# Kernel optimization log

Hardware: AMD Instinct MI355X
Metric: run time of the kernel (lower is better)

## Reference

```python
import jax, jax.numpy as jnp
import numpy as np

N_NODES = 50000
N_EDGES = 800000
D = 128
L = 4
N_GRAPHS = 512
N_CLASSES = 10
BN_EPS = 1e-5


def setup_inputs() -> dict:
    key = jax.random.key(0)
    ks = jax.random.split(key, 8)
    x = jax.random.normal(ks[0], (N_NODES, D), dtype=jnp.float32)
    W = jax.random.normal(ks[1], (L, D, D), dtype=jnp.float32) * (1.0 / np.sqrt(D))
    b = jnp.zeros((L, D), dtype=jnp.float32)
    gamma = jnp.ones((L, D), dtype=jnp.float32)
    beta = jnp.zeros((L, D), dtype=jnp.float32)
    Wc = jax.random.normal(ks[2], (D, N_CLASSES), dtype=jnp.float32) * (1.0 / np.sqrt(D))
    bc = jnp.zeros((N_CLASSES,), dtype=jnp.float32)
    edge_index = jax.random.randint(ks[3], (2, N_EDGES), 0, N_NODES, dtype=jnp.int64)
    batch = jnp.sort(jax.random.randint(ks[4], (N_NODES,), 0, N_GRAPHS, dtype=jnp.int64))
    return {"x": x, "W": W, "b": b, "gamma": gamma, "beta": beta,
            "Wc": Wc, "bc": bc, "edge_index": edge_index, "batch": batch}


def _gcn_conv(x, W_l, b_l, src, dst, deg_inv, norm):
    # h = x @ W, then symmetric-normalized aggregation with self-loops (PyG GCNConv)
    h = x @ W_l                                            # [N, D]
    msg = h[src] * norm[:, None]                           # [E, D] gather + scale
    agg = jax.ops.segment_sum(msg, dst, num_segments=N_NODES)  # scatter-add
    agg = agg + h * (deg_inv * deg_inv)[:, None]           # self-loop term: deg^-1 * h_i
    return agg + b_l


def reference(x, W, b, gamma, beta, Wc, bc, edge_index, batch):
    src, dst = edge_index[0], edge_index[1]
    # degree with self-loops (edge_weight = 1), computed at target nodes
    deg = jax.ops.segment_sum(jnp.ones((N_EDGES,), x.dtype), dst, num_segments=N_NODES) + 1.0
    deg_inv = deg ** -0.5                                  # [N]
    norm = deg_inv[src] * deg_inv[dst]                     # [E]
    for l in range(L):
        x = _gcn_conv(x, W[l], b[l], src, dst, deg_inv, norm)
        # BatchNorm1d (training-mode statistics, biased variance) + ReLU
        mu = jnp.mean(x, axis=0)
        var = jnp.mean((x - mu) ** 2, axis=0)
        x = (x - mu) * jax.lax.rsqrt(var + BN_EPS) * gamma[l] + beta[l]
        x = jax.nn.relu(x)
        # dropout omitted (eval-mode / deterministic reference)
    # global mean pool over graphs, then classifier
    sums = jax.ops.segment_sum(x, batch, num_segments=N_GRAPHS)          # [G, D]
    counts = jax.ops.segment_sum(jnp.ones((N_NODES,), x.dtype), batch, num_segments=N_GRAPHS)
    pooled = sums / jnp.maximum(counts, 1.0)[:, None]
    return pooled @ Wc + bc                                # [G, num_classes]
```

## Files before the change

### kernel.cpp

```cpp
#include <hip/hip_runtime.h>
#include <hip/hip_bf16.h>

#define N_NODES 50000
#define N_EDGES 800000
#define D 128
#define NLAYERS 4
#define N_GRAPHS 512
#define N_CLASSES 10
#define BN_EPS 1e-5f

__global__ void k_hist(const int* __restrict__ ei, int* __restrict__ counts) {
    int e = blockIdx.x * blockDim.x + threadIdx.x;
    if (e < N_EDGES) atomicAdd(&counts[ei[N_EDGES + e]], 1);
}

__global__ void k_scan(const int* __restrict__ counts, int* __restrict__ offsets,
                       float* __restrict__ deg_inv) {
    __shared__ int wsum[16];
    __shared__ int s_run;
    int tid = threadIdx.x, lane = tid & 63, wid = tid >> 6;
    if (tid == 0) { s_run = 0; offsets[0] = 0; }
    __syncthreads();
    for (int base = 0; base < N_NODES; base += 1024) {
        int i = base + tid;
        int v = (i < N_NODES) ? counts[i] : 0;
        if (i < N_NODES) deg_inv[i] = rsqrtf((float)v + 1.0f);
        int x = v;
        #pragma unroll
        for (int off = 1; off < 64; off <<= 1) {
            int y = __shfl_up(x, off, 64);
            if (lane >= off) x += y;
        }
        if (lane == 63) wsum[wid] = x;
        __syncthreads();
        if (wid == 0 && lane < 16) {
            int w = wsum[lane];
            #pragma unroll
            for (int off = 1; off < 16; off <<= 1) {
                int y = __shfl_up(w, off, 16);
                if ((lane & 15) >= off) w += y;
            }
            wsum[lane] = w;
        }
        __syncthreads();
        int wbase = (wid > 0) ? wsum[wid - 1] : 0;
        int incl = x + wbase;
        int run = s_run;
        if (i < N_NODES) offsets[i + 1] = run + incl;
        __syncthreads();
        if (tid == 1023) s_run = run + incl;
        __syncthreads();
    }
}

__global__ void k_scatter(const int* __restrict__ ei, const int* __restrict__ offsets,
                          int* __restrict__ cursor, const float* __restrict__ deg_inv,
                          int2* __restrict__ csr) {
    int e = blockIdx.x * blockDim.x + threadIdx.x;
    if (e >= N_EDGES) return;
    int s = ei[e];
    int d = ei[N_EDGES + e];
    int pos = offsets[d] + atomicAdd(&cursor[d], 1);
    csr[pos] = make_int2(s, __float_as_int(deg_inv[s] * deg_inv[d]));
}

#define GEMM_BM 64
__global__ __launch_bounds__(256) void k_gemm(const float* __restrict__ X,
                                              const float* __restrict__ Wl,
                                              float* __restrict__ H,
                                              const float* __restrict__ gstats,
                                              const float* __restrict__ gamma,
                                              const float* __restrict__ beta,
                                              int do_bn_relu) {
    __shared__ float xs[GEMM_BM][D];
    __shared__ float s_sc[D], s_sh[D];
    int tid = threadIdx.x;
    if (tid < D) {
        if (do_bn_relu) {
            const float invN = 1.0f / (float)N_NODES;
            float mu = gstats[tid] * invN;
            float var = gstats[D + tid] * invN - mu * mu;
            float sc = gamma[tid] * rsqrtf(var + BN_EPS);
            s_sc[tid] = sc;
            s_sh[tid] = beta[tid] - mu * sc;
        } else {
            s_sc[tid] = 1.0f;
            s_sh[tid] = 0.0f;
        }
    }
    __syncthreads();
    int row0 = blockIdx.x * GEMM_BM;
    #pragma unroll
    for (int j = 0; j < 8; j++) {
        int idx = tid + j * 256;
        int r = idx >> 5;
        int c4 = (idx & 31) * 4;
        float4 v;
        int gr = row0 + r;
        if (gr < N_NODES) v = *(const float4*)&X[(long)gr * D + c4];
        else v = make_float4(0.f, 0.f, 0.f, 0.f);
        if (do_bn_relu) {
            v.x = fmaxf(v.x * s_sc[c4 + 0] + s_sh[c4 + 0], 0.f);
            v.y = fmaxf(v.y * s_sc[c4 + 1] + s_sh[c4 + 1], 0.f);
            v.z = fmaxf(v.z * s_sc[c4 + 2] + s_sh[c4 + 2], 0.f);
            v.w = fmaxf(v.w * s_sc[c4 + 3] + s_sh[c4 + 3], 0.f);
        }
        *(float4*)&xs[r][c4] = v;
    }
    __syncthreads();
    int tc = tid & 31, tr = tid >> 5;
    int r0 = tr * 8, c0 = tc * 4;
    float acc[8][4] = {};
    #pragma unroll 4
    for (int k = 0; k < D; k++) {
        float4 w = *(const float4*)&Wl[k * D + c0];
        #pragma unroll
        for (int i = 0; i < 8; i++) {
            float xv = xs[r0 + i][k];
            acc[i][0] += xv * w.x;
            acc[i][1] += xv * w.y;
            acc[i][2] += xv * w.z;
            acc[i][3] += xv * w.w;
        }
    }
    #pragma unroll
    for (int i = 0; i < 8; i++) {
        int gr = row0 + r0 + i;
        if (gr < N_NODES) {
            float4 o = make_float4(acc[i][0], acc[i][1], acc[i][2], acc[i][3]);
            *(float4*)&H[(long)gr * D + c0] = o;
        }
    }
}

#define AGG_NPW 8
#define AGG_WAVES 4
__global__ __launch_bounds__(256) void k_agg(const float* __restrict__ H,
                                             const float* __restrict__ deg_inv,
                                             const int* __restrict__ offsets,
                                             const int2* __restrict__ csr,
                                             const float* __restrict__ bias,
                                             float* __restrict__ Xout,
                                             float* __restrict__ gsum,
                                             float* __restrict__ gsq) {
    __shared__ float s_sum[D], s_sq[D];
    int tid = threadIdx.x, lane = tid & 63, wid = tid >> 6;
    if (tid < D) { s_sum[tid] = 0.f; s_sq[tid] = 0.f; }
    __syncthreads();
    int c = lane * 2;
    float b0 = bias[c], b1 = bias[c + 1];
    float ps0 = 0.f, ps1 = 0.f, pq0 = 0.f, pq1 = 0.f;
    int nodeBase = blockIdx.x * (AGG_NPW * AGG_WAVES) + wid * AGG_NPW;
    for (int t = 0; t < AGG_NPW; t++) {
        int n = nodeBase + t;
        if (n >= N_NODES) break;
        float di = deg_inv[n];
        float2 hv = *(const float2*)&H[(long)n * D + c];
        float self = di * di;
        float a0 = hv.x * self + b0;
        float a1 = hv.y * self + b1;
        int e = offsets[n], e1 = offsets[n + 1];
        for (; e + 4 <= e1; e += 4) {
            int2 p0 = csr[e + 0];
            int2 p1 = csr[e + 1];
            int2 p2 = csr[e + 2];
            int2 p3 = csr[e + 3];
            float2 h0 = *(const float2*)&H[(long)p0.x * D + c];
            float2 h1 = *(const float2*)&H[(long)p1.x * D + c];
            float2 h2 = *(const float2*)&H[(long)p2.x * D + c];
            float2 h3 = *(const float2*)&H[(long)p3.x * D + c];
            float w0 = __int_as_float(p0.y), w1 = __int_as_float(p1.y);
            float w2 = __int_as_float(p2.y), w3 = __int_as_float(p3.y);
            a0 += h0.x * w0; a1 += h0.y * w0;
            a0 += h1.x * w1; a1 += h1.y * w1;
            a0 += h2.x * w2; a1 += h2.y * w2;
            a0 += h3.x * w3; a1 += h3.y * w3;
        }
        for (; e < e1; e++) {
            int2 p = csr[e];
            float w = __int_as_float(p.y);
            float2 hs = *(const float2*)&H[(long)p.x * D + c];
            a0 += hs.x * w;
            a1 += hs.y * w;
        }
        *(float2*)&Xout[(long)n * D + c] = make_float2(a0, a1);
        ps0 += a0; ps1 += a1;
        pq0 += a0 * a0; pq1 += a1 * a1;
    }
    atomicAdd(&s_sum[c], ps0);
    atomicAdd(&s_sum[c + 1], ps1);
    atomicAdd(&s_sq[c], pq0);
    atomicAdd(&s_sq[c + 1], pq1);
    __syncthreads();
    if (tid < D) {
        atomicAdd(&gsum[tid], s_sum[tid]);
        atomicAdd(&gsq[tid], s_sq[tid]);
    }
}

__global__ __launch_bounds__(128) void k_poolcls(const float* __restrict__ X,
                                                 const int* __restrict__ batch,
                                                 const float* __restrict__ gstats,
                                                 const float* __restrict__ gamma,
                                                 const float* __restrict__ beta,
                                                 const float* __restrict__ Wc,
                                                 const float* __restrict__ bc,
                                                 float* __restrict__ out) {
    __shared__ float s_pool[D];
    __shared__ int s_lo, s_hi;
    int g = blockIdx.x, tid = threadIdx.x;
    if (tid == 0) {
        int lo = 0, hi = N_NODES;
        while (lo < hi) { int m = (lo + hi) >> 1; if (batch[m] < g) lo = m + 1; else hi = m; }
        s_lo = lo;
        lo = s_lo; hi = N_NODES;
        while (lo < hi) { int m = (lo + hi) >> 1; if (batch[m] < g + 1) lo = m + 1; else hi = m; }
        s_hi = lo;
    }
    __syncthreads();
    int lo = s_lo, hi = s_hi;
    const float invN = 1.0f / (float)N_NODES;
    float mu = gstats[tid] * invN;
    float var = gstats[D + tid] * invN - mu * mu;
    float sc = gamma[tid] * rsqrtf(var + BN_EPS);
    float sh = beta[tid] - mu * sc;
    float acc = 0.f;
    for (int n = lo; n < hi; n++) {
        float v = X[(long)n * D + tid];
        acc += fmaxf(v * sc + sh, 0.f);
    }
    float cnt = fmaxf((float)(hi - lo), 1.0f);
    s_pool[tid] = acc / cnt;
    __syncthreads();
    if (tid < N_CLASSES) {
        float r = bc[tid];
        #pragma unroll 16
        for (int k = 0; k < D; k++) r += s_pool[k] * Wc[k * N_CLASSES + tid];
        out[(long)g * N_CLASSES + tid] = r;
    }
}

extern "C" void kernel_launch(void* const* d_in, const int* in_sizes, int n_in,
                              void* d_out, int out_size, void* d_ws, size_t ws_size,
                              hipStream_t stream) {
    const float* x     = (const float*)d_in[0];
    const float* W     = (const float*)d_in[1];
    const float* b     = (const float*)d_in[2];
    const float* gamma = (const float*)d_in[3];
    const float* beta  = (const float*)d_in[4];
    const float* Wc    = (const float*)d_in[5];
    const float* bc    = (const float*)d_in[6];
    const int*   ei    = (const int*)d_in[7];
    const int*   batch = (const int*)d_in[8];
    float* out = (float*)d_out;

    char* ws = (char*)d_ws;
    size_t off = 0;
    auto alloc = [&](size_t bytes) {
        void* p = ws + off;
        off += (bytes + 255) & ~(size_t)255;
        return p;
    };
    float* cur_x    = (float*)alloc((size_t)N_NODES * D * 4);
    float* h        = (float*)alloc((size_t)N_NODES * D * 4);
    float* deg_inv  = (float*)alloc(N_NODES * 4);
    int*   offsets  = (int*)alloc((N_NODES + 1) * 4);
    int2*  csr      = (int2*)alloc((size_t)N_EDGES * 8);
    size_t zero_begin = off;
    int*   counts   = (int*)alloc(N_NODES * 4);
    int*   cursor   = (int*)alloc(N_NODES * 4);
    float* gstats   = (float*)alloc((size_t)NLAYERS * 2 * D * 4);
    size_t zero_end = off;

    hipMemsetAsync(ws + zero_begin, 0, zero_end - zero_begin, stream);

    k_hist<<<(N_EDGES + 255) / 256, 256, 0, stream>>>(ei, counts);
    k_scan<<<1, 1024, 0, stream>>>(counts, offsets, deg_inv);
    k_scatter<<<(N_EDGES + 255) / 256, 256, 0, stream>>>(ei, offsets, cursor, deg_inv, csr);

    const int gemm_grid = (N_NODES + GEMM_BM - 1) / GEMM_BM;
    const int agg_grid = (N_NODES + AGG_NPW * AGG_WAVES - 1) / (AGG_NPW * AGG_WAVES);
    for (int l = 0; l < NLAYERS; l++) {
        const float* Xin = (l == 0) ? x : cur_x;
        const float* st  = (l == 0) ? nullptr : gstats + (size_t)(l - 1) * 2 * D;
        const float* gm  = gamma + (size_t)((l == 0) ? 0 : l - 1) * D;
        const float* bt  = beta + (size_t)((l == 0) ? 0 : l - 1) * D;
        k_gemm<<<gemm_grid, 256, 0, stream>>>(Xin, W + (size_t)l * D * D, h,
                                              st, gm, bt, (l == 0) ? 0 : 1);
        float* gs = gstats + (size_t)l * 2 * D;
        k_agg<<<agg_grid, 256, 0, stream>>>(h, deg_inv, offsets, csr,
                                            b + (size_t)l * D, cur_x, gs, gs + D);
    }

    k_poolcls<<<N_GRAPHS, 128, 0, stream>>>(cur_x, batch,
                                            gstats + (size_t)(NLAYERS - 1) * 2 * D,
                                            gamma + (size_t)(NLAYERS - 1) * D,
                                            beta + (size_t)(NLAYERS - 1) * D,
                                            Wc, bc, out);
}
```

Before: 751.2 us.

## Parallelize degree scan, shrink aggregation per-wave work, vectorize pooling kernel

Replaces the single-block serial prefix scan over 50k nodes with a two-pass multi-block scan (per-block scan plus block-prefix fixup). Reduces nodes per wave in the aggregation kernel from 8 to 2, so many more blocks launch and load balance improves. In exchange, each block now issues its stats atomics for fewer nodes. Rewrites pooling to use 256 threads with float4 loads and row-strided accumulation, combined through shared atomics, and moves the division by the node count after the classifier.

```diff
diff --git a/kernel.cpp b/kernel.cpp
--- a/kernel.cpp
+++ b/kernel.cpp
@@ -8,49 +8,59 @@
 #define N_GRAPHS 512
 #define N_CLASSES 10
 #define BN_EPS 1e-5f
+#define SCAN_BLOCKS ((N_NODES + 1023) / 1024)
 
 __global__ void k_hist(const int* __restrict__ ei, int* __restrict__ counts) {
     int e = blockIdx.x * blockDim.x + threadIdx.x;
     if (e < N_EDGES) atomicAdd(&counts[ei[N_EDGES + e]], 1);
 }
 
-__global__ void k_scan(const int* __restrict__ counts, int* __restrict__ offsets,
-                       float* __restrict__ deg_inv) {
+__global__ __launch_bounds__(1024) void k_scan1(const int* __restrict__ counts,
+                                                int* __restrict__ offsets,
+                                                float* __restrict__ deg_inv,
+                                                int* __restrict__ bsum) {
     __shared__ int wsum[16];
-    __shared__ int s_run;
     int tid = threadIdx.x, lane = tid & 63, wid = tid >> 6;
-    if (tid == 0) { s_run = 0; offsets[0] = 0; }
-    __syncthreads();
-    for (int base = 0; base < N_NODES; base += 1024) {
-        int i = base + tid;
-        int v = (i < N_NODES) ? counts[i] : 0;
-        if (i < N_NODES) deg_inv[i] = rsqrtf((float)v + 1.0f);
-        int x = v;
+    int i = blockIdx.x * 1024 + tid;
+    int v = (i < N_NODES) ? counts[i] : 0;
+    if (i < N_NODES) deg_inv[i] = rsqrtf((float)v + 1.0f);
+    int x = v;
+    #pragma unroll
+    for (int off = 1; off < 64; off <<= 1) {
+        int y = __shfl_up(x, off, 64);
+        if (lane >= off) x += y;
+    }
+    if (lane == 63) wsum[wid] = x;
+    __syncthreads();
+    if (wid == 0 && lane < 16) {
+        int w = wsum[lane];
         #pragma unroll
-        for (int off = 1; off < 64; off <<= 1) {
-            int y = __shfl_up(x, off, 64);
-            if (lane >= off) x += y;
-        }
-        if (lane == 63) wsum[wid] = x;
-        __syncthreads();
-        if (wid == 0 && lane < 16) {
-            int w = wsum[lane];
-            #pragma unroll
-            for (int off = 1; off < 16; off <<= 1) {
-                int y = __shfl_up(w, off, 16);
-                if ((lane & 15) >= off) w += y;
-            }
-            wsum[lane] = w;
-        }
-        __syncthreads();
-        int wbase = (wid > 0) ? wsum[wid - 1] : 0;
-        int incl = x + wbase;
-        int run = s_run;
-        if (i < N_NODES) offsets[i + 1] = run + incl;
-        __syncthreads();
-        if (tid == 1023) s_run = run + incl;
-        __syncthreads();
-    }
+        for (int off = 1; off < 16; off <<= 1) {
+            int y = __shfl_up(w, off, 16);
+            if (lane >= off) w += y;
+        }
+        wsum[lane] = w;
+    }
+    __syncthreads();
+    int wbase = (wid > 0) ? wsum[wid - 1] : 0;
+    int incl = x + wbase;
+    if (i < N_NODES) offsets[i + 1] = incl;
+    if (tid == 1023) bsum[blockIdx.x] = incl;
+}
+
+__global__ __launch_bounds__(1024) void k_scan2(int* __restrict__ offsets,
+                                                const int* __restrict__ bsum) {
+    __shared__ int s_pre;
+    int b = blockIdx.x, tid = threadIdx.x;
+    if (tid == 0) {
+        int p = 0;
+        for (int j = 0; j < b; j++) p += bsum[j];
+        s_pre = p;
+        if (b == 0) offsets[0] = 0;
+    }
+    __syncthreads();
+    int i = b * 1024 + tid;
+    if (i < N_NODES) offsets[i + 1] += s_pre;
 }
 
 __global__ void k_scatter(const int* __restrict__ ei, const int* __restrict__ offsets,
@@ -133,8 +143,9 @@
     }
 }
 
-#define AGG_NPW 8
+#define AGG_NPW 2
 #define AGG_WAVES 4
+#define AGG_NPB (AGG_NPW * AGG_WAVES)
 __global__ __launch_bounds__(256) void k_agg(const float* __restrict__ H,
                                              const float* __restrict__ deg_inv,
                                              const int* __restrict__ offsets,
@@ -150,7 +161,7 @@
     int c = lane * 2;
     float b0 = bias[c], b1 = bias[c + 1];
     float ps0 = 0.f, ps1 = 0.f, pq0 = 0.f, pq1 = 0.f;
-    int nodeBase = blockIdx.x * (AGG_NPW * AGG_WAVES) + wid * AGG_NPW;
+    int nodeBase = blockIdx.x * AGG_NPB + wid * AGG_NPW;
     for (int t = 0; t < AGG_NPW; t++) {
         int n = nodeBase + t;
         if (n >= N_NODES) break;
@@ -198,7 +209,7 @@
     }
 }
 
-__global__ __launch_bounds__(128) void k_poolcls(const float* __restrict__ X,
+__global__ __launch_bounds__(256) void k_poolcls(const float* __restrict__ X,
                                                  const int* __restrict__ batch,
                                                  const float* __restrict__ gstats,
                                                  const float* __restrict__ gamma,
@@ -213,30 +224,40 @@
         int lo = 0, hi = N_NODES;
         while (lo < hi) { int m = (lo + hi) >> 1; if (batch[m] < g) lo = m + 1; else hi = m; }
         s_lo = lo;
-        lo = s_lo; hi = N_NODES;
+        hi = N_NODES;
         while (lo < hi) { int m = (lo + hi) >> 1; if (batch[m] < g + 1) lo = m + 1; else hi = m; }
         s_hi = lo;
     }
+    if (tid < D) s_pool[tid] = 0.f;
     __syncthreads();
     int lo = s_lo, hi = s_hi;
+    int c4 = (tid & 31) * 4, q = tid >> 5;
     const float invN = 1.0f / (float)N_NODES;
-    float mu = gstats[tid] * invN;
-    float var = gstats[D + tid] * invN - mu * mu;
-    float sc = gamma[tid] * rsqrtf(var + BN_EPS);
-    float sh = beta[tid] - mu * sc;
-    float acc = 0.f;
-    for (int n = lo; n < hi; n++) {
-        float v = X[(long)n * D + tid];
-        acc += fmaxf(v * sc + sh, 0.f);
-    }
-    float cnt = fmaxf((float)(hi - lo), 1.0f);
-    s_pool[tid] = acc / cnt;
+    float sc[4], sh[4];
+    #pragma unroll
+    for (int j = 0; j < 4; j++) {
+        float mu = gstats[c4 + j] * invN;
+        float var = gstats[D + c4 + j] * invN - mu * mu;
+        sc[j] = gamma[c4 + j] * rsqrtf(var + BN_EPS);
+        sh[j] = beta[c4 + j] - mu * sc[j];
+    }
+    float acc[4] = {0.f, 0.f, 0.f, 0.f};
+    for (int n = lo + q; n < hi; n += 8) {
+        float4 v = *(const float4*)&X[(long)n * D + c4];
+        acc[0] += fmaxf(v.x * sc[0] + sh[0], 0.f);
+        acc[1] += fmaxf(v.y * sc[1] + sh[1], 0.f);
+        acc[2] += fmaxf(v.z * sc[2] + sh[2], 0.f);
+        acc[3] += fmaxf(v.w * sc[3] + sh[3], 0.f);
+    }
+    #pragma unroll
+    for (int j = 0; j < 4; j++) atomicAdd(&s_pool[c4 + j], acc[j]);
     __syncthreads();
     if (tid < N_CLASSES) {
-        float r = bc[tid];
+        float cnt = fmaxf((float)(hi - lo), 1.0f);
+        float r = 0.f;
         #pragma unroll 16
         for (int k = 0; k < D; k++) r += s_pool[k] * Wc[k * N_CLASSES + tid];
-        out[(long)g * N_CLASSES + tid] = r;
+        out[(long)g * N_CLASSES + tid] = r / cnt + bc[tid];
     }
 }
 
@@ -266,6 +287,7 @@
     float* deg_inv  = (float*)alloc(N_NODES * 4);
     int*   offsets  = (int*)alloc((N_NODES + 1) * 4);
     int2*  csr      = (int2*)alloc((size_t)N_EDGES * 8);
+    int*   bsum     = (int*)alloc(SCAN_BLOCKS * 4);
     size_t zero_begin = off;
     int*   counts   = (int*)alloc(N_NODES * 4);
     int*   cursor   = (int*)alloc(N_NODES * 4);
@@ -275,11 +297,12 @@
     hipMemsetAsync(ws + zero_begin, 0, zero_end - zero_begin, stream);
 
     k_hist<<<(N_EDGES + 255) / 256, 256, 0, stream>>>(ei, counts);
-    k_scan<<<1, 1024, 0, stream>>>(counts, offsets, deg_inv);
+    k_scan1<<<SCAN_BLOCKS, 1024, 0, stream>>>(counts, offsets, deg_inv, bsum);
+    k_scan2<<<SCAN_BLOCKS, 1024, 0, stream>>>(offsets, bsum);
     k_scatter<<<(N_EDGES + 255) / 256, 256, 0, stream>>>(ei, offsets, cursor, deg_inv, csr);
 
     const int gemm_grid = (N_NODES + GEMM_BM - 1) / GEMM_BM;
-    const int agg_grid = (N_NODES + AGG_NPW * AGG_WAVES - 1) / (AGG_NPW * AGG_WAVES);
+    const int agg_grid = (N_NODES + AGG_NPB - 1) / AGG_NPB;
     for (int l = 0; l < NLAYERS; l++) {
         const float* Xin = (l == 0) ? x : cur_x;
         const float* st  = (l == 0) ? nullptr : gstats + (size_t)(l - 1) * 2 * D;
@@ -292,7 +315,7 @@
                                             b + (size_t)l * D, cur_x, gs, gs + D);
     }
 
-    k_poolcls<<<N_GRAPHS, 128, 0, stream>>>(cur_x, batch,
+    k_poolcls<<<N_GRAPHS, 256, 0, stream>>>(cur_x, batch,
                                             gstats + (size_t)(NLAYERS - 1) * 2 * D,
                                             gamma + (size_t)(NLAYERS - 1) * D,
                                             beta + (size_t)(NLAYERS - 1) * D,
```

New measurement: 1.058 ms. 1.41x slower.
